# Optimization experiments

Hardware: AMD Instinct MI355X
Metric: run time of the kernel (lower is better)

The kernel has to match this reference:

```python
import jax, jax.numpy as jnp
import numpy as np

B, T, IN, OUT = 32, 1024, 1024, 1024
DT = 1.0
TAU_MIN, TAU_MAX = 5.0, 25.0


def setup_inputs() -> dict:
    key = jax.random.key(0)
    k1, k2, k3 = jax.random.split(key, 3)
    bound = 1.0 / np.sqrt(IN)
    inputs = jax.random.normal(k1, (B, T, IN), dtype=jnp.float32)
    weight = jax.random.uniform(k2, (OUT, IN), dtype=jnp.float32, minval=-bound, maxval=bound)
    bias = jnp.zeros((OUT,), dtype=jnp.float32)
    # per-neuron decay alpha = exp(-dt/tau), tau ~ U[tau_min, tau_max]
    tau = jax.random.uniform(k3, (OUT,), dtype=jnp.float32, minval=TAU_MIN, maxval=TAU_MAX)
    decay = jnp.exp(-DT / tau)
    return {"inputs": inputs, "weight": weight, "bias": bias, "decay": decay}


def reference(inputs, weight, bias, decay):
    # time-distributed linear projection: [B,T,IN] @ [OUT,IN]^T -> [B,T,OUT]
    current = jnp.einsum('bti,oi->bto', inputs, weight) + bias
    u0 = jnp.zeros((inputs.shape[0], weight.shape[0]), dtype=current.dtype)

    def step(u, x_t):
        # leaky integrator: u_t = alpha*u_{t-1} + (1-alpha)*x_t
        u = decay * u + (1.0 - decay) * x_t
        return u, u

    # scan over time: move T to leading axis
    _, u_seq = jax.lax.scan(step, u0, jnp.swapaxes(current, 0, 1))
    return jnp.swapaxes(u_seq, 0, 1)  # [B,T,OUT]
```

## Files before the change

kernel.cpp:

```cpp
#include <hip/hip_runtime.h>

#define M_DIM 32768
#define N_DIM 1024
#define K_DIM 1024
#define T_DIM 1024
#define B_DIM 32
#define NCHUNK 8
#define CHUNK_T 128

typedef unsigned int uint32;
typedef __attribute__((ext_vector_type(8))) short short8;
typedef __attribute__((ext_vector_type(8))) unsigned short ushort8v;
typedef __attribute__((ext_vector_type(4))) float floatx4;

__device__ __forceinline__ unsigned short f2bf(float f) {
    uint32 u = __float_as_uint(f);
    uint32 r = u + 0x7fffu + ((u >> 16) & 1u);
    return (unsigned short)(r >> 16);
}

__device__ __forceinline__ void async_load16(const void* g, void* s) {
    __builtin_amdgcn_global_load_lds(
        (const __attribute__((address_space(1))) void*)g,
        (__attribute__((address_space(3))) void*)s,
        16, 0, 0);
}

__global__ void cast_f32_bf16_x8(const float* __restrict__ src,
                                 unsigned short* __restrict__ dst, int n8) {
    int i = blockIdx.x * blockDim.x + threadIdx.x;
    if (i < n8) {
        const float4* s4 = (const float4*)src;
        float4 v0 = s4[(size_t)i * 2];
        float4 v1 = s4[(size_t)i * 2 + 1];
        ushort8v o;
        o[0] = f2bf(v0.x); o[1] = f2bf(v0.y); o[2] = f2bf(v0.z); o[3] = f2bf(v0.w);
        o[4] = f2bf(v1.x); o[5] = f2bf(v1.y); o[6] = f2bf(v1.z); o[7] = f2bf(v1.w);
        ((ushort8v*)dst)[i] = o;
    }
}

__global__ __launch_bounds__(512, 2) void gemm_8phase(
    const unsigned short* __restrict__ A,
    const unsigned short* __restrict__ Bw,
    const float* __restrict__ bias,
    unsigned short* __restrict__ outBf) {
    extern __shared__ __align__(16) unsigned short smem[];

    const int tid  = threadIdx.x;
    const int lane = tid & 63;
    const int wid  = tid >> 6;
    const int l15  = lane & 15;
    const int quad = lane >> 4;
    const int wm   = wid >> 2;
    const int wn   = wid & 3;

    const int L   = blockIdx.y * gridDim.x + blockIdx.x;
    const int xcd = L & 7;
    const int s   = L >> 3;
    const int bn0 = (s & 3) * 256;
    const int bm0 = (xcd * 16 + (s >> 2)) * 256;

    const int t3  = tid >> 3;
    const int sc8 = ((tid & 7) ^ (t3 & 7)) * 8;

#define STAGE_A(IH, T, PB) do {                                              \
        size_t kof_ = (size_t)(T) * 64 + sc8;                                \
        _Pragma("unroll") for (int q_ = 0; q_ < 2; ++q_) {                   \
            int ar_ = q_ * 128 + (IH) * 64 + t3;                             \
            int dr_ = q_ * 128 + (IH) * 64 + wid * 8;                        \
            async_load16(A + (size_t)(bm0 + ar_) * K_DIM + kof_,             \
                         smem + (PB) * 32768 + dr_ * 64);                    \
        } } while (0)
#define STAGE_B(JH, T, PB) do {                                              \
        size_t kof_ = (size_t)(T) * 64 + sc8;                                \
        _Pragma("unroll") for (int q_ = 0; q_ < 2; ++q_) {                   \
            int br_ = (q_ * 2 + (tid >> 8)) * 64 + (JH) * 32 + (t3 & 31);    \
            int dr_ = (q_ * 2 + (wid >> 2)) * 64 + (JH) * 32 + (wid & 3) * 8;\
            async_load16(Bw + (size_t)(bn0 + br_) * K_DIM + kof_,            \
                         smem + (PB) * 32768 + 16384 + dr_ * 64);            \
        } } while (0)

#define LD_A(IH) do {                                                        \
        const unsigned short* As_ = smem + pb * 32768;                       \
        _Pragma("unroll") for (int ii = 0; ii < 4; ++ii) {                   \
            int r_ = wm * 128 + (IH) * 64 + ii * 16 + l15;                   \
            _Pragma("unroll") for (int ks = 0; ks < 2; ++ks) {               \
                int c_ = ks * 4 + quad;                                      \
                af[ii][ks] = *(const short8*)&As_[r_ * 64 +                  \
                                                 ((c_ ^ (l15 & 7)) * 8)];    \
            } } } while (0)
#define LD_B(JH) do {                                                        \
        const unsigned short* Bs_ = smem + pb * 32768 + 16384;               \
        _Pragma("unroll") for (int jj = 0; jj < 2; ++jj) {                   \
            int r_ = wn * 64 + ((JH) * 2 + jj) * 16 + l15;                   \
            _Pragma("unroll") for (int ks = 0; ks < 2; ++ks) {               \
                int c_ = ks * 4 + quad;                                      \
                bfr[(JH) * 2 + jj][ks] = *(const short8*)&Bs_[r_ * 64 +      \
                                                 ((c_ ^ (l15 & 7)) * 8)];    \
            } } } while (0)
#define MM(IH, JH) do {                                                      \
        __builtin_amdgcn_s_setprio(1);                                       \
        _Pragma("unroll") for (int ii = 0; ii < 4; ++ii)                     \
        _Pragma("unroll") for (int jj = 0; jj < 2; ++jj)                     \
        _Pragma("unroll") for (int ks = 0; ks < 2; ++ks)                     \
            acc[(IH) * 4 + ii][(JH) * 2 + jj] =                              \
                __builtin_amdgcn_mfma_f32_16x16x32_bf16(                     \
                    af[ii][ks], bfr[(JH) * 2 + jj][ks],                      \
                    acc[(IH) * 4 + ii][(JH) * 2 + jj], 0, 0, 0);             \
        __builtin_amdgcn_s_setprio(0);                                       \
    } while (0)

#define FENCE  asm volatile("" ::: "memory")
#define BAR    __builtin_amdgcn_s_barrier()
#define LGKM0  asm volatile("s_waitcnt lgkmcnt(0)" ::: "memory")
#define SCHED0 __builtin_amdgcn_sched_barrier(0)

    floatx4 acc[8][4];
#pragma unroll
    for (int i = 0; i < 8; ++i)
#pragma unroll
        for (int j = 0; j < 4; ++j)
            acc[i][j] = (floatx4){0.f, 0.f, 0.f, 0.f};

    short8 af[4][2];
    short8 bfr[4][2];

    const int NT = K_DIM / 64;

    STAGE_A(0, 0, 0); STAGE_A(1, 0, 0); STAGE_B(0, 0, 0); STAGE_B(1, 0, 0);
    STAGE_A(0, 1, 1); STAGE_B(1, 1, 1); STAGE_B(0, 1, 1);
    asm volatile("s_waitcnt vmcnt(6)" ::: "memory");
    FENCE; BAR;

    for (int g = 0; g < NT; ++g) {
        const int pb = g & 1;
        const int po = pb ^ 1;

        LD_A(0); LD_B(0);
        if (g + 1 < NT) STAGE_A(1, g + 1, po);
        FENCE; BAR; LGKM0; SCHED0;
        MM(0, 0);
        SCHED0; FENCE; BAR;

        LD_B(1);
        if (g + 2 < NT) STAGE_A(0, g + 2, pb);
        FENCE; BAR; LGKM0; SCHED0;
        MM(0, 1);
        SCHED0; FENCE; BAR;

        LD_A(1);
        if (g + 2 < NT) STAGE_B(1, g + 2, pb);
        FENCE; BAR; LGKM0; SCHED0;
        MM(1, 0);
        SCHED0; FENCE; BAR;

        if (g + 2 < NT) STAGE_B(0, g + 2, pb);
        if (g < NT - 2) {
            asm volatile("s_waitcnt vmcnt(6)" ::: "memory");
        } else if (g == NT - 2) {
            asm volatile("s_waitcnt vmcnt(0)" ::: "memory");
        }
        FENCE; BAR; LGKM0; SCHED0;
        MM(1, 1);
        SCHED0; FENCE; BAR;
    }
    asm volatile("s_waitcnt vmcnt(0)" ::: "memory");

    float bb[4];
#pragma unroll
    for (int j = 0; j < 4; ++j) bb[j] = bias[bn0 + wn * 64 + j * 16 + l15];
#pragma unroll
    for (int i = 0; i < 8; ++i) {
        int rowb = bm0 + wm * 128 + i * 16 + quad * 4;
#pragma unroll
        for (int r = 0; r < 4; ++r) {
            size_t rb = (size_t)(rowb + r) * N_DIM + bn0 + wn * 64 + l15;
#pragma unroll
            for (int j = 0; j < 4; ++j)
                outBf[rb + j * 16] = f2bf(acc[i][j][r] + bb[j]);
        }
    }
#undef STAGE_A
#undef STAGE_B
#undef LD_A
#undef LD_B
#undef MM
#undef FENCE
#undef BAR
#undef LGKM0
#undef SCHED0
}

__global__ __launch_bounds__(256) void gemm_mfma(
    const unsigned short* __restrict__ A,
    const unsigned short* __restrict__ Bw,
    const float* __restrict__ bias,
    unsigned short* outBf,
    float* outF) {
    __shared__ unsigned short As[128 * 64];
    __shared__ unsigned short Bs[128 * 64];

    const int tid  = threadIdx.x;
    const int lane = tid & 63;
    const int wid  = tid >> 6;
    const int l15  = lane & 15;
    const int quad = lane >> 4;
    const int wm   = wid >> 1;
    const int wn   = wid & 1;

    const int L    = blockIdx.y * gridDim.x + blockIdx.x;
    const int xcd  = L & 7;
    const int s    = L >> 3;
    const int bn0  = (s & 7) * 128;
    const int bm0  = (xcd * 32 + (s >> 3)) * 128;

    floatx4 acc[4][4];
#pragma unroll
    for (int i = 0; i < 4; ++i)
#pragma unroll
        for (int j = 0; j < 4; ++j)
            acc[i][j] = (floatx4){0.f, 0.f, 0.f, 0.f};

    for (int kt = 0; kt < K_DIM / 64; ++kt) {
        const int k0 = kt * 64;
#pragma unroll
        for (int q = 0; q < 4; ++q) {
            int slot = q * 256 + tid;
            int row  = slot >> 3;
            int chq  = slot & 7;
            int scq  = chq ^ (row & 7);
            async_load16(A + (size_t)(bm0 + row) * K_DIM + k0 + scq * 8,
                         &As[(q * 256 + wid * 64) * 8]);
        }
#pragma unroll
        for (int q = 0; q < 4; ++q) {
            int slot = q * 256 + tid;
            int row  = slot >> 3;
            int chq  = slot & 7;
            int scq  = chq ^ (row & 7);
            async_load16(Bw + (size_t)(bn0 + row) * K_DIM + k0 + scq * 8,
                         &Bs[(q * 256 + wid * 64) * 8]);
        }
        __syncthreads();

#pragma unroll
        for (int ks = 0; ks < 2; ++ks) {
            short8 af[4], bfr[4];
#pragma unroll
            for (int i = 0; i < 4; ++i) {
                int r = wm * 64 + i * 16 + l15;
                int c = ks * 4 + quad;
                af[i] = *(const short8*)&As[r * 64 + ((c ^ (r & 7)) * 8)];
            }
#pragma unroll
            for (int j = 0; j < 4; ++j) {
                int r = wn * 64 + j * 16 + l15;
                int c = ks * 4 + quad;
                bfr[j] = *(const short8*)&Bs[r * 64 + ((c ^ (r & 7)) * 8)];
            }
#pragma unroll
            for (int i = 0; i < 4; ++i)
#pragma unroll
                for (int j = 0; j < 4; ++j)
                    acc[i][j] = __builtin_amdgcn_mfma_f32_16x16x32_bf16(
                        af[i], bfr[j], acc[i][j], 0, 0, 0);
        }
        __syncthreads();
    }

#pragma unroll
    for (int j = 0; j < 4; ++j) {
        int col = bn0 + wn * 64 + j * 16 + l15;
        float bb = bias[col];
#pragma unroll
        for (int i = 0; i < 4; ++i) {
            int rowb = bm0 + wm * 64 + i * 16 + quad * 4;
#pragma unroll
            for (int r = 0; r < 4; ++r) {
                float v = acc[i][j][r] + bb;
                size_t idx = (size_t)(rowb + r) * N_DIM + col;
                if (outBf) outBf[idx] = f2bf(v);
                else       outF[idx]  = v;
            }
        }
    }
}

__global__ __launch_bounds__(256) void scan_carry2(
    const uint32* __restrict__ cur32,
    const float* __restrict__ decay,
    float* __restrict__ carry) {
    int tid   = blockIdx.x * 256 + threadIdx.x;
    int o2    = tid & 511;
    int chunk = (tid >> 9) & (NCHUNK - 1);
    int b     = tid >> 12;
    int o     = o2 * 2;
    size_t base = ((size_t)b * T_DIM + (size_t)chunk * CHUNK_T) * (N_DIM / 2) + o2;
    float2 a2 = *(const float2*)&decay[o];
    float a0 = a2.x, a1 = a2.y;
    float c0 = 1.f - a0, c1 = 1.f - a1;
    float u0 = 0.f, u1 = 0.f;
    for (int t0 = 0; t0 < CHUNK_T; t0 += 32) {
        uint32 x[32];
#pragma unroll
        for (int k = 0; k < 32; ++k)
            x[k] = cur32[base + (size_t)(t0 + k) * (N_DIM / 2)];
#pragma unroll
        for (int k = 0; k < 32; ++k) {
            float lo = __uint_as_float(x[k] << 16);
            float hi = __uint_as_float(x[k] & 0xffff0000u);
            u0 = a0 * u0 + c0 * lo;
            u1 = a1 * u1 + c1 * hi;
        }
    }
    float2* cw = (float2*)&carry[((size_t)b * NCHUNK + chunk) * N_DIM + o];
    *cw = (float2){u0, u1};
}

__global__ __launch_bounds__(256) void scan_apply2(
    const uint32* __restrict__ cur32,
    const float* __restrict__ decay,
    const float* __restrict__ carry,
    float* __restrict__ out) {
    int tid   = blockIdx.x * 256 + threadIdx.x;
    int o2    = tid & 511;
    int chunk = (tid >> 9) & (NCHUNK - 1);
    int b     = tid >> 12;
    int o     = o2 * 2;
    size_t base = ((size_t)b * T_DIM + (size_t)chunk * CHUNK_T) * (N_DIM / 2) + o2;
    float2 a2 = *(const float2*)&decay[o];
    float a0 = a2.x, a1 = a2.y;
    float c0 = 1.f - a0, c1 = 1.f - a1;

    float A0 = a0, A1 = a1;
#pragma unroll
    for (int i = 0; i < 7; ++i) { A0 *= A0; A1 *= A1; }

    float u0 = 0.f, u1 = 0.f;
    const float* cb = carry + (size_t)b * NCHUNK * N_DIM + o;
    for (int i = 0; i < chunk; ++i) {
        float2 cv = *(const float2*)&cb[(size_t)i * N_DIM];
        u0 = cv.x + A0 * u0;
        u1 = cv.y + A1 * u1;
    }

    float2* out2 = (float2*)out;
    size_t obase = ((size_t)b * T_DIM + (size_t)chunk * CHUNK_T) * (N_DIM / 2) + o2;
    for (int t0 = 0; t0 < CHUNK_T; t0 += 32) {
        uint32 x[32];
#pragma unroll
        for (int k = 0; k < 32; ++k)
            x[k] = cur32[base + (size_t)(t0 + k) * (N_DIM / 2)];
#pragma unroll
        for (int k = 0; k < 32; ++k) {
            float lo = __uint_as_float(x[k] << 16);
            float hi = __uint_as_float(x[k] & 0xffff0000u);
            u0 = a0 * u0 + c0 * lo;
            u1 = a1 * u1 + c1 * hi;
            out2[obase + (size_t)(t0 + k) * (N_DIM / 2)] = (float2){u0, u1};
        }
    }
}

__global__ void scan_f32_inplace(float* __restrict__ buf,
                                 const float* __restrict__ decay) {
    int tid = blockIdx.x * 64 + threadIdx.x;
    int o = tid & (N_DIM - 1);
    size_t base = ((size_t)(tid >> 10) << 20) + o;
    float a = decay[o];
    float c = 1.f - a;
    float u = 0.f;
    for (int t0 = 0; t0 < 1024; t0 += 16) {
        float x[16];
#pragma unroll
        for (int k = 0; k < 16; ++k)
            x[k] = buf[base + (size_t)(t0 + k) * N_DIM];
#pragma unroll
        for (int k = 0; k < 16; ++k) {
            u = a * u + c * x[k];
            buf[base + (size_t)(t0 + k) * N_DIM] = u;
        }
    }
}

__global__ void gemm_naive(const float* __restrict__ X, const float* __restrict__ W,
                           const float* __restrict__ bias, float* __restrict__ out) {
    __shared__ float As[16][17], Bs[16][17];
    int tx = threadIdx.x, ty = threadIdx.y;
    int m0 = blockIdx.y * 16, n0 = blockIdx.x * 16;
    float acc = 0.f;
    for (int k0 = 0; k0 < K_DIM; k0 += 16) {
        As[ty][tx] = X[(size_t)(m0 + ty) * K_DIM + k0 + tx];
        Bs[ty][tx] = W[(size_t)(n0 + ty) * K_DIM + k0 + tx];
        __syncthreads();
#pragma unroll
        for (int kk = 0; kk < 16; ++kk) acc += As[ty][kk] * Bs[tx][kk];
        __syncthreads();
    }
    out[(size_t)(m0 + ty) * N_DIM + n0 + tx] = acc + bias[n0 + tx];
}

extern "C" void kernel_launch(void* const* d_in, const int* in_sizes, int n_in,
                              void* d_out, int out_size, void* d_ws, size_t ws_size,
                              hipStream_t stream) {
    const float* X     = (const float*)d_in[0];
    const float* Wt    = (const float*)d_in[1];
    const float* bias  = (const float*)d_in[2];
    const float* decay = (const float*)d_in[3];
    float* out = (float*)d_out;

    static bool big_lds_ok = [] {
        return hipFuncSetAttribute(reinterpret_cast<const void*>(gemm_8phase),
                                   hipFuncAttributeMaxDynamicSharedMemorySize,
                                   131072) == hipSuccess;
    }();

    const size_t A_bytes  = (size_t)M_DIM * K_DIM * 2;
    const size_t W_bytes  = (size_t)N_DIM * K_DIM * 2;
    const size_t C_bytes  = (size_t)M_DIM * N_DIM * 2;
    const size_t cr_bytes = (size_t)B_DIM * NCHUNK * N_DIM * 4;
    const size_t need_mid  = A_bytes + W_bytes;
    const size_t need_full = A_bytes + W_bytes + C_bytes + cr_bytes;

    if (ws_size >= need_full) {
        unsigned short* Abf = (unsigned short*)d_ws;
        unsigned short* Wbf = (unsigned short*)((char*)d_ws + A_bytes);
        unsigned short* Cbf = (unsigned short*)((char*)d_ws + A_bytes + W_bytes);
        float* carry = (float*)((char*)d_ws + A_bytes + W_bytes + C_bytes);
        cast_f32_bf16_x8<<<(M_DIM * K_DIM / 8 + 255) / 256, 256, 0, stream>>>(X, Abf, M_DIM * K_DIM / 8);
        cast_f32_bf16_x8<<<(N_DIM * K_DIM / 8 + 255) / 256, 256, 0, stream>>>(Wt, Wbf, N_DIM * K_DIM / 8);
        if (big_lds_ok) {
            gemm_8phase<<<dim3(4, 128), 512, 131072, stream>>>(Abf, Wbf, bias, Cbf);
        } else {
            gemm_mfma<<<dim3(N_DIM / 128, M_DIM / 128), 256, 0, stream>>>(Abf, Wbf, bias, Cbf, nullptr);
        }
        const int scan_threads = B_DIM * NCHUNK * N_DIM / 2;
        scan_carry2<<<scan_threads / 256, 256, 0, stream>>>((const uint32*)Cbf, decay, carry);
        scan_apply2<<<scan_threads / 256, 256, 0, stream>>>((const uint32*)Cbf, decay, carry, out);
    } else if (ws_size >= need_mid) {
        unsigned short* Abf = (unsigned short*)d_ws;
        unsigned short* Wbf = (unsigned short*)((char*)d_ws + A_bytes);
        cast_f32_bf16_x8<<<(M_DIM * K_DIM / 8 + 255) / 256, 256, 0, stream>>>(X, Abf, M_DIM * K_DIM / 8);
        cast_f32_bf16_x8<<<(N_DIM * K_DIM / 8 + 255) / 256, 256, 0, stream>>>(Wt, Wbf, N_DIM * K_DIM / 8);
        gemm_mfma<<<dim3(N_DIM / 128, M_DIM / 128), 256, 0, stream>>>(Abf, Wbf, bias, nullptr, out);
        scan_f32_inplace<<<512, 64, 0, stream>>>(out, decay);
    } else {
        gemm_naive<<<dim3(N_DIM / 16, M_DIM / 16), dim3(16, 16), 0, stream>>>(X, Wt, bias, out);
        scan_f32_inplace<<<512, 64, 0, stream>>>(out, decay);
    }
}
```

Before: 154.9 us.

## Fuse fp32-to-bf16 input cast into a triple-buffered GEMM reading fp32 activations

```diff
diff --git a/kernel.cpp b/kernel.cpp
--- a/kernel.cpp
+++ b/kernel.cpp
@@ -24,6 +24,15 @@
         (const __attribute__((address_space(1))) void*)g,
         (__attribute__((address_space(3))) void*)s,
         16, 0, 0);
+}
+
+__device__ __forceinline__ short8 pk8(float4 a, float4 b) {
+    union { short8 s; uint32 d[4]; } u;
+    asm("v_cvt_pk_bf16_f32 %0, %1, %2" : "=v"(u.d[0]) : "v"(a.x), "v"(a.y));
+    asm("v_cvt_pk_bf16_f32 %0, %1, %2" : "=v"(u.d[1]) : "v"(a.z), "v"(a.w));
+    asm("v_cvt_pk_bf16_f32 %0, %1, %2" : "=v"(u.d[2]) : "v"(b.x), "v"(b.y));
+    asm("v_cvt_pk_bf16_f32 %0, %1, %2" : "=v"(u.d[3]) : "v"(b.z), "v"(b.w));
+    return u.s;
 }
 
 __global__ void cast_f32_bf16_x8(const float* __restrict__ src,
@@ -38,6 +47,145 @@
         o[4] = f2bf(v1.x); o[5] = f2bf(v1.y); o[6] = f2bf(v1.z); o[7] = f2bf(v1.w);
         ((ushort8v*)dst)[i] = o;
     }
+}
+
+__global__ __launch_bounds__(512, 2) void gemm_f32a(
+    const float* __restrict__ X32,
+    const unsigned short* __restrict__ Bw,
+    const float* __restrict__ bias,
+    unsigned short* __restrict__ outBf) {
+    extern __shared__ __align__(16) char smemc[];
+
+    const int tid  = threadIdx.x;
+    const int lane = tid & 63;
+    const int wid  = tid >> 6;
+    const int l15  = lane & 15;
+    const int quad = lane >> 4;
+    const int wm   = wid >> 2;
+    const int wn   = wid & 3;
+
+    const int L   = blockIdx.y * gridDim.x + blockIdx.x;
+    const int xcd = L & 7;
+    const int s   = L >> 3;
+    const int bn0 = (s & 3) * 256;
+    const int bm0 = (xcd * 16 + (s >> 2)) * 256;
+
+#define STAGE_A_U(U, T, PB) do {                                             \
+        int row_ = (U) * 64 + (tid >> 3);                                    \
+        int sc_  = ((tid & 7) ^ (row_ & 7)) * 4;                             \
+        async_load16(X32 + (size_t)(bm0 + row_) * K_DIM + (T) * 32 + sc_,    \
+                     (float*)smemc + (PB) * 8192 + ((U) * 64 + wid * 8) * 32); \
+    } while (0)
+#define STAGE_B_U(U, T, PB) do {                                             \
+        int row_ = (U) * 128 + (tid >> 2);                                   \
+        int sc_  = ((tid & 3) ^ (row_ & 3)) * 8;                             \
+        async_load16(Bw + (size_t)(bn0 + row_) * K_DIM + (T) * 32 + sc_,     \
+                     (unsigned short*)(smemc + 98304) + (PB) * 8192 +        \
+                         ((U) * 128 + wid * 16) * 32);                       \
+    } while (0)
+
+#define LD_A(IH) do {                                                        \
+        const float* As_ = (const float*)smemc + pb * 8192;                  \
+        _Pragma("unroll") for (int ii = 0; ii < 4; ++ii) {                   \
+            int r_ = wm * 128 + (IH) * 64 + ii * 16 + l15;                   \
+            int k_ = l15 & 7;                                                \
+            int c0_ = quad * 2;                                              \
+            float4 F0 = *(const float4*)&As_[r_ * 32 + ((c0_ ^ k_) * 4)];    \
+            float4 F1 = *(const float4*)&As_[r_ * 32 + (((c0_ + 1) ^ k_) * 4)]; \
+            af[ii] = pk8(F0, F1);                                            \
+        } } while (0)
+#define LD_B() do {                                                          \
+        const unsigned short* Bs_ =                                          \
+            (const unsigned short*)(smemc + 98304) + pb * 8192;              \
+        _Pragma("unroll") for (int jj = 0; jj < 4; ++jj) {                   \
+            int r_ = wn * 64 + jj * 16 + l15;                                \
+            bfr[jj] = *(const short8*)&Bs_[r_ * 32 + ((quad ^ (l15 & 3)) * 8)]; \
+        } } while (0)
+#define MM(IH) do {                                                          \
+        __builtin_amdgcn_s_setprio(1);                                       \
+        _Pragma("unroll") for (int ii = 0; ii < 4; ++ii)                     \
+        _Pragma("unroll") for (int jj = 0; jj < 4; ++jj)                     \
+            acc[(IH) * 4 + ii][jj] =                                         \
+                __builtin_amdgcn_mfma_f32_16x16x32_bf16(                     \
+                    af[ii], bfr[jj], acc[(IH) * 4 + ii][jj], 0, 0, 0);       \
+        __builtin_amdgcn_s_setprio(0);                                       \
+    } while (0)
+
+#define FENCE  asm volatile("" ::: "memory")
+#define BAR    __builtin_amdgcn_s_barrier()
+#define LGKM0  asm volatile("s_waitcnt lgkmcnt(0)" ::: "memory")
+#define SCHED0 __builtin_amdgcn_sched_barrier(0)
+
+    floatx4 acc[8][4];
+#pragma unroll
+    for (int i = 0; i < 8; ++i)
+#pragma unroll
+        for (int j = 0; j < 4; ++j)
+            acc[i][j] = (floatx4){0.f, 0.f, 0.f, 0.f};
+
+    short8 af[4];
+    short8 bfr[4];
+
+    const int NT = K_DIM / 32;
+
+    STAGE_A_U(0, 0, 0); STAGE_A_U(1, 0, 0); STAGE_A_U(2, 0, 0); STAGE_A_U(3, 0, 0);
+    STAGE_B_U(0, 0, 0); STAGE_B_U(1, 0, 0);
+    STAGE_A_U(0, 1, 1); STAGE_A_U(1, 1, 1); STAGE_A_U(2, 1, 1); STAGE_A_U(3, 1, 1);
+    STAGE_B_U(0, 1, 1); STAGE_B_U(1, 1, 1);
+    asm volatile("s_waitcnt vmcnt(6)" ::: "memory");
+    FENCE; BAR;
+
+    int pb = 0;
+    for (int g = 0; g < NT; ++g) {
+        const int pn = (pb >= 1) ? pb - 1 : 2;
+
+        LD_A(0); LD_B();
+        if (g + 2 < NT) { STAGE_A_U(0, g + 2, pn); STAGE_A_U(1, g + 2, pn);
+                          STAGE_A_U(2, g + 2, pn); }
+        FENCE; BAR; LGKM0; SCHED0;
+        MM(0);
+        SCHED0; FENCE; BAR;
+
+        LD_A(1);
+        if (g + 2 < NT) { STAGE_A_U(3, g + 2, pn); STAGE_B_U(0, g + 2, pn);
+                          STAGE_B_U(1, g + 2, pn); }
+        if (g < NT - 2) {
+            asm volatile("s_waitcnt vmcnt(6)" ::: "memory");
+        } else if (g == NT - 2) {
+            asm volatile("s_waitcnt vmcnt(0)" ::: "memory");
+        }
+        FENCE; BAR; LGKM0; SCHED0;
+        MM(1);
+        SCHED0; FENCE; BAR;
+
+        pb = (pb == 2) ? 0 : pb + 1;
+    }
+    asm volatile("s_waitcnt vmcnt(0)" ::: "memory");
+
+    float bb[4];
+#pragma unroll
+    for (int j = 0; j < 4; ++j) bb[j] = bias[bn0 + wn * 64 + j * 16 + l15];
+    unsigned short* eb = (unsigned short*)smemc + wid * 2048;
+#pragma unroll
+    for (int i = 0; i < 8; ++i) {
+#pragma unroll
+        for (int j = 0; j < 4; ++j)
+#pragma unroll
+            for (int r = 0; r < 4; ++r)
+                eb[(quad * 4 + r) * 64 + j * 16 + l15] = f2bf(acc[i][j][r] + bb[j]);
+        asm volatile("s_waitcnt lgkmcnt(0)" ::: "memory");
+        short8 v0 = *(const short8*)&eb[lane * 8];
+        short8 v1 = *(const short8*)&eb[512 + lane * 8];
+        int rowg = bm0 + wm * 128 + i * 16 + (lane >> 3);
+        int colg = bn0 + wn * 64 + (lane & 7) * 8;
+        *(short8*)&outBf[(size_t)rowg * N_DIM + colg] = v0;
+        *(short8*)&outBf[(size_t)(rowg + 8) * N_DIM + colg] = v1;
+    }
+#undef STAGE_A_U
+#undef STAGE_B_U
+#undef LD_A
+#undef LD_B
+#undef MM
 }
 
 __global__ __launch_bounds__(512, 2) void gemm_8phase(
@@ -80,8 +228,7 @@
             async_load16(Bw + (size_t)(bn0 + br_) * K_DIM + kof_,            \
                          smem + (PB) * 32768 + 16384 + dr_ * 64);            \
         } } while (0)
-
-#define LD_A(IH) do {                                                        \
+#define LD_A8(IH) do {                                                       \
         const unsigned short* As_ = smem + pb * 32768;                       \
         _Pragma("unroll") for (int ii = 0; ii < 4; ++ii) {                   \
             int r_ = wm * 128 + (IH) * 64 + ii * 16 + l15;                   \
@@ -90,7 +237,7 @@
                 af[ii][ks] = *(const short8*)&As_[r_ * 64 +                  \
                                                  ((c_ ^ (l15 & 7)) * 8)];    \
             } } } while (0)
-#define LD_B(JH) do {                                                        \
+#define LD_B8(JH) do {                                                       \
         const unsigned short* Bs_ = smem + pb * 32768 + 16384;               \
         _Pragma("unroll") for (int jj = 0; jj < 2; ++jj) {                   \
             int r_ = wn * 64 + ((JH) * 2 + jj) * 16 + l15;                   \
@@ -99,7 +246,7 @@
                 bfr[(JH) * 2 + jj][ks] = *(const short8*)&Bs_[r_ * 64 +      \
                                                  ((c_ ^ (l15 & 7)) * 8)];    \
             } } } while (0)
-#define MM(IH, JH) do {                                                      \
+#define MM8(IH, JH) do {                                                     \
         __builtin_amdgcn_s_setprio(1);                                       \
         _Pragma("unroll") for (int ii = 0; ii < 4; ++ii)                     \
         _Pragma("unroll") for (int jj = 0; jj < 2; ++jj)                     \
@@ -111,11 +258,6 @@
         __builtin_amdgcn_s_setprio(0);                                       \
     } while (0)
 
-#define FENCE  asm volatile("" ::: "memory")
-#define BAR    __builtin_amdgcn_s_barrier()
-#define LGKM0  asm volatile("s_waitcnt lgkmcnt(0)" ::: "memory")
-#define SCHED0 __builtin_amdgcn_sched_barrier(0)
-
     floatx4 acc[8][4];
 #pragma unroll
     for (int i = 0; i < 8; ++i)
@@ -137,22 +279,22 @@
         const int pb = g & 1;
         const int po = pb ^ 1;
 
-        LD_A(0); LD_B(0);
+        LD_A8(0); LD_B8(0);
         if (g + 1 < NT) STAGE_A(1, g + 1, po);
         FENCE; BAR; LGKM0; SCHED0;
-        MM(0, 0);
+        MM8(0, 0);
         SCHED0; FENCE; BAR;
 
-        LD_B(1);
+        LD_B8(1);
         if (g + 2 < NT) STAGE_A(0, g + 2, pb);
         FENCE; BAR; LGKM0; SCHED0;
-        MM(0, 1);
+        MM8(0, 1);
         SCHED0; FENCE; BAR;
 
-        LD_A(1);
+        LD_A8(1);
         if (g + 2 < NT) STAGE_B(1, g + 2, pb);
         FENCE; BAR; LGKM0; SCHED0;
-        MM(1, 0);
+        MM8(1, 0);
         SCHED0; FENCE; BAR;
 
         if (g + 2 < NT) STAGE_B(0, g + 2, pb);
@@ -162,7 +304,7 @@
             asm volatile("s_waitcnt vmcnt(0)" ::: "memory");
         }
         FENCE; BAR; LGKM0; SCHED0;
-        MM(1, 1);
+        MM8(1, 1);
         SCHED0; FENCE; BAR;
     }
     asm volatile("s_waitcnt vmcnt(0)" ::: "memory");
@@ -183,108 +325,13 @@
     }
 #undef STAGE_A
 #undef STAGE_B
-#undef LD_A
-#undef LD_B
-#undef MM
+#undef LD_A8
+#undef LD_B8
+#undef MM8
 #undef FENCE
 #undef BAR
 #undef LGKM0
 #undef SCHED0
-}
-
-__global__ __launch_bounds__(256) void gemm_mfma(
-    const unsigned short* __restrict__ A,
-    const unsigned short* __restrict__ Bw,
-    const float* __restrict__ bias,
-    unsigned short* outBf,
-    float* outF) {
-    __shared__ unsigned short As[128 * 64];
-    __shared__ unsigned short Bs[128 * 64];
-
-    const int tid  = threadIdx.x;
-    const int lane = tid & 63;
-    const int wid  = tid >> 6;
-    const int l15  = lane & 15;
-    const int quad = lane >> 4;
-    const int wm   = wid >> 1;
-    const int wn   = wid & 1;
-
-    const int L    = blockIdx.y * gridDim.x + blockIdx.x;
-    const int xcd  = L & 7;
-    const int s    = L >> 3;
-    const int bn0  = (s & 7) * 128;
-    const int bm0  = (xcd * 32 + (s >> 3)) * 128;
-
-    floatx4 acc[4][4];
-#pragma unroll
-    for (int i = 0; i < 4; ++i)
-#pragma unroll
-        for (int j = 0; j < 4; ++j)
-            acc[i][j] = (floatx4){0.f, 0.f, 0.f, 0.f};
-
-    for (int kt = 0; kt < K_DIM / 64; ++kt) {
-        const int k0 = kt * 64;
-#pragma unroll
-        for (int q = 0; q < 4; ++q) {
-            int slot = q * 256 + tid;
-            int row  = slot >> 3;
-            int chq  = slot & 7;
-            int scq  = chq ^ (row & 7);
-            async_load16(A + (size_t)(bm0 + row) * K_DIM + k0 + scq * 8,
-                         &As[(q * 256 + wid * 64) * 8]);
-        }
-#pragma unroll
-        for (int q = 0; q < 4; ++q) {
-            int slot = q * 256 + tid;
-            int row  = slot >> 3;
-            int chq  = slot & 7;
-            int scq  = chq ^ (row & 7);
-            async_load16(Bw + (size_t)(bn0 + row) * K_DIM + k0 + scq * 8,
-                         &Bs[(q * 256 + wid * 64) * 8]);
-        }
-        __syncthreads();
-
-#pragma unroll
-        for (int ks = 0; ks < 2; ++ks) {
-            short8 af[4], bfr[4];
-#pragma unroll
-            for (int i = 0; i < 4; ++i) {
-                int r = wm * 64 + i * 16 + l15;
-                int c = ks * 4 + quad;
-                af[i] = *(const short8*)&As[r * 64 + ((c ^ (r & 7)) * 8)];
-            }
-#pragma unroll
-            for (int j = 0; j < 4; ++j) {
-                int r = wn * 64 + j * 16 + l15;
-                int c = ks * 4 + quad;
-                bfr[j] = *(const short8*)&Bs[r * 64 + ((c ^ (r & 7)) * 8)];
-            }
-#pragma unroll
-            for (int i = 0; i < 4; ++i)
-#pragma unroll
-                for (int j = 0; j < 4; ++j)
-                    acc[i][j] = __builtin_amdgcn_mfma_f32_16x16x32_bf16(
-                        af[i], bfr[j], acc[i][j], 0, 0, 0);
-        }
-        __syncthreads();
-    }
-
-#pragma unroll
-    for (int j = 0; j < 4; ++j) {
-        int col = bn0 + wn * 64 + j * 16 + l15;
-        float bb = bias[col];
-#pragma unroll
-        for (int i = 0; i < 4; ++i) {
-            int rowb = bm0 + wm * 64 + i * 16 + quad * 4;
-#pragma unroll
-            for (int r = 0; r < 4; ++r) {
-                float v = acc[i][j][r] + bb;
-                size_t idx = (size_t)(rowb + r) * N_DIM + col;
-                if (outBf) outBf[idx] = f2bf(v);
-                else       outF[idx]  = v;
-            }
-        }
-    }
 }
 
 __global__ __launch_bounds__(256) void scan_carry2(
@@ -384,6 +431,101 @@
     }
 }
 
+__global__ __launch_bounds__(256) void gemm_mfma(
+    const unsigned short* __restrict__ A,
+    const unsigned short* __restrict__ Bw,
+    const float* __restrict__ bias,
+    unsigned short* outBf,
+    float* outF) {
+    __shared__ unsigned short As[128 * 64];
+    __shared__ unsigned short Bs[128 * 64];
+
+    const int tid  = threadIdx.x;
+    const int lane = tid & 63;
+    const int wid  = tid >> 6;
+    const int l15  = lane & 15;
+    const int quad = lane >> 4;
+    const int wm   = wid >> 1;
+    const int wn   = wid & 1;
+
+    const int L    = blockIdx.y * gridDim.x + blockIdx.x;
+    const int xcd  = L & 7;
+    const int s    = L >> 3;
+    const int bn0  = (s & 7) * 128;
+    const int bm0  = (xcd * 32 + (s >> 3)) * 128;
+
+    floatx4 acc[4][4];
+#pragma unroll
+    for (int i = 0; i < 4; ++i)
+#pragma unroll
+        for (int j = 0; j < 4; ++j)
+            acc[i][j] = (floatx4){0.f, 0.f, 0.f, 0.f};
+
+    for (int kt = 0; kt < K_DIM / 64; ++kt) {
+        const int k0 = kt * 64;
+#pragma unroll
+        for (int q = 0; q < 4; ++q) {
+            int slot = q * 256 + tid;
+            int row  = slot >> 3;
+            int chq  = slot & 7;
+            int scq  = chq ^ (row & 7);
+            async_load16(A + (size_t)(bm0 + row) * K_DIM + k0 + scq * 8,
+                         &As[(q * 256 + wid * 64) * 8]);
+        }
+#pragma unroll
+        for (int q = 0; q < 4; ++q) {
+            int slot = q * 256 + tid;
+            int row  = slot >> 3;
+            int chq  = slot & 7;
+            int scq  = chq ^ (row & 7);
+            async_load16(Bw + (size_t)(bn0 + row) * K_DIM + k0 + scq * 8,
+                         &Bs[(q * 256 + wid * 64) * 8]);
+        }
+        __syncthreads();
+
+#pragma unroll
+        for (int ks = 0; ks < 2; ++ks) {
+            short8 af[4], bfr[4];
+#pragma unroll
+            for (int i = 0; i < 4; ++i) {
+                int r = wm * 64 + i * 16 + l15;
+                int c = ks * 4 + quad;
+                af[i] = *(const short8*)&As[r * 64 + ((c ^ (r & 7)) * 8)];
+            }
+#pragma unroll
+            for (int j = 0; j < 4; ++j) {
+                int r = wn * 64 + j * 16 + l15;
+                int c = ks * 4 + quad;
+                bfr[j] = *(const short8*)&Bs[r * 64 + ((c ^ (r & 7)) * 8)];
+            }
+#pragma unroll
+            for (int i = 0; i < 4; ++i)
+#pragma unroll
+                for (int j = 0; j < 4; ++j)
+                    acc[i][j] = __builtin_amdgcn_mfma_f32_16x16x32_bf16(
+                        af[i], bfr[j], acc[i][j], 0, 0, 0);
+        }
+        __syncthreads();
+    }
+
+#pragma unroll
+    for (int j = 0; j < 4; ++j) {
+        int col = bn0 + wn * 64 + j * 16 + l15;
+        float bb = bias[col];
+#pragma unroll
+        for (int i = 0; i < 4; ++i) {
+            int rowb = bm0 + wm * 64 + i * 16 + quad * 4;
+#pragma unroll
+            for (int r = 0; r < 4; ++r) {
+                float v = acc[i][j][r] + bb;
+                size_t idx = (size_t)(rowb + r) * N_DIM + col;
+                if (outBf) outBf[idx] = f2bf(v);
+                else       outF[idx]  = v;
+            }
+        }
+    }
+}
+
 __global__ void gemm_naive(const float* __restrict__ X, const float* __restrict__ W,
                            const float* __restrict__ bias, float* __restrict__ out) {
     __shared__ float As[16][17], Bs[16][17];
@@ -410,7 +552,12 @@
     const float* decay = (const float*)d_in[3];
     float* out = (float*)d_out;
 
-    static bool big_lds_ok = [] {
+    static bool lds144_ok = [] {
+        return hipFuncSetAttribute(reinterpret_cast<const void*>(gemm_f32a),
+                                   hipFuncAttributeMaxDynamicSharedMemorySize,
+                                   147456) == hipSuccess;
+    }();
+    static bool lds128_ok = [] {
         return hipFuncSetAttribute(reinterpret_cast<const void*>(gemm_8phase),
                                    hipFuncAttributeMaxDynamicSharedMemorySize,
                                    131072) == hipSuccess;
@@ -420,22 +567,27 @@
     const size_t W_bytes  = (size_t)N_DIM * K_DIM * 2;
     const size_t C_bytes  = (size_t)M_DIM * N_DIM * 2;
     const size_t cr_bytes = (size_t)B_DIM * NCHUNK * N_DIM * 4;
+    const size_t need_new  = W_bytes + C_bytes + cr_bytes;
     const size_t need_mid  = A_bytes + W_bytes;
     const size_t need_full = A_bytes + W_bytes + C_bytes + cr_bytes;
-
-    if (ws_size >= need_full) {
+    const int scan_threads = B_DIM * NCHUNK * N_DIM / 2;
+
+    if (lds144_ok && ws_size >= need_new) {
+        unsigned short* Wbf = (unsigned short*)d_ws;
+        unsigned short* Cbf = (unsigned short*)((char*)d_ws + W_bytes);
+        float* carry = (float*)((char*)d_ws + W_bytes + C_bytes);
+        cast_f32_bf16_x8<<<(N_DIM * K_DIM / 8 + 255) / 256, 256, 0, stream>>>(Wt, Wbf, N_DIM * K_DIM / 8);
+        gemm_f32a<<<dim3(4, 128), 512, 147456, stream>>>(X, Wbf, bias, Cbf);
+        scan_carry2<<<scan_threads / 256, 256, 0, stream>>>((const uint32*)Cbf, decay, carry);
+        scan_apply2<<<scan_threads / 256, 256, 0, stream>>>((const uint32*)Cbf, decay, carry, out);
+    } else if (lds128_ok && ws_size >= need_full) {
         unsigned short* Abf = (unsigned short*)d_ws;
         unsigned short* Wbf = (unsigned short*)((char*)d_ws + A_bytes);
         unsigned short* Cbf = (unsigned short*)((char*)d_ws + A_bytes + W_bytes);
         float* carry = (float*)((char*)d_ws + A_bytes + W_bytes + C_bytes);
         cast_f32_bf16_x8<<<(M_DIM * K_DIM / 8 + 255) / 256, 256, 0, stream>>>(X, Abf, M_DIM * K_DIM / 8);
         cast_f32_bf16_x8<<<(N_DIM * K_DIM / 8 + 255) / 256, 256, 0, stream>>>(Wt, Wbf, N_DIM * K_DIM / 8);
-        if (big_lds_ok) {
-            gemm_8phase<<<dim3(4, 128), 512, 131072, stream>>>(Abf, Wbf, bias, Cbf);
-        } else {
-            gemm_mfma<<<dim3(N_DIM / 128, M_DIM / 128), 256, 0, stream>>>(Abf, Wbf, bias, Cbf, nullptr);
-        }
-        const int scan_threads = B_DIM * NCHUNK * N_DIM / 2;
+        gemm_8phase<<<dim3(4, 128), 512, 131072, stream>>>(Abf, Wbf, bias, Cbf);
         scan_carry2<<<scan_threads / 256, 256, 0, stream>>>((const uint32*)Cbf, decay, carry);
         scan_apply2<<<scan_threads / 256, 256, 0, stream>>>((const uint32*)Cbf, decay, carry, out);
     } else if (ws_size >= need_mid) {
```

Measured after the change: 174.8 us. +12.8%, slower.

## Fuse fp32-to-bf16 activation cast into GEMM A-tile staging

Applied to the files above, without the earlier changes.

```diff
diff --git a/kernel.cpp b/kernel.cpp
--- a/kernel.cpp
+++ b/kernel.cpp
@@ -25,6 +25,74 @@
         (__attribute__((address_space(3))) void*)s,
         16, 0, 0);
 }
+
+__device__ __forceinline__ short8 pk8(floatx4 a, floatx4 b) {
+    union { short8 s; uint32 d[4]; } u;
+    asm("v_cvt_pk_bf16_f32 %0, %1, %2" : "=v"(u.d[0]) : "v"(a[0]), "v"(a[1]));
+    asm("v_cvt_pk_bf16_f32 %0, %1, %2" : "=v"(u.d[1]) : "v"(a[2]), "v"(a[3]));
+    asm("v_cvt_pk_bf16_f32 %0, %1, %2" : "=v"(u.d[2]) : "v"(b[0]), "v"(b[1]));
+    asm("v_cvt_pk_bf16_f32 %0, %1, %2" : "=v"(u.d[3]) : "v"(b[2]), "v"(b[3]));
+    return u.s;
+}
+
+#define FENCE  asm volatile("" ::: "memory")
+#define BAR    __builtin_amdgcn_s_barrier()
+#define LGKM0  asm volatile("s_waitcnt lgkmcnt(0)" ::: "memory")
+#define SCHED0 __builtin_amdgcn_sched_barrier(0)
+#define VMW(N) asm volatile("s_waitcnt vmcnt(" #N ")" ::: "memory")
+
+#define STAGE_B(JH, T, PB) do {                                              \
+        size_t kof_ = (size_t)(T) * 64 + sc8;                                \
+        _Pragma("unroll") for (int q_ = 0; q_ < 2; ++q_) {                   \
+            int br_ = (q_ * 2 + (tid >> 8)) * 64 + (JH) * 32 + (t3 & 31);    \
+            int dr_ = (q_ * 2 + (wid >> 2)) * 64 + (JH) * 32 + (wid & 3) * 8;\
+            async_load16(Bw + (size_t)(bn0 + br_) * K_DIM + kof_,            \
+                         smem + (PB) * 32768 + 16384 + dr_ * 64);            \
+        } } while (0)
+
+#define LD_A8(IH) do {                                                       \
+        const unsigned short* As_ = smem + pb * 32768;                       \
+        _Pragma("unroll") for (int ii = 0; ii < 4; ++ii) {                   \
+            int r_ = wm * 128 + (IH) * 64 + ii * 16 + l15;                   \
+            _Pragma("unroll") for (int ks = 0; ks < 2; ++ks) {               \
+                int c_ = ks * 4 + quad;                                      \
+                af[ii][ks] = *(const short8*)&As_[r_ * 64 +                  \
+                                                 ((c_ ^ (l15 & 7)) * 8)];    \
+            } } } while (0)
+#define LD_B8(JH) do {                                                       \
+        const unsigned short* Bs_ = smem + pb * 32768 + 16384;               \
+        _Pragma("unroll") for (int jj = 0; jj < 2; ++jj) {                   \
+            int r_ = wn * 64 + ((JH) * 2 + jj) * 16 + l15;                   \
+            _Pragma("unroll") for (int ks = 0; ks < 2; ++ks) {               \
+                int c_ = ks * 4 + quad;                                      \
+                bfr[(JH) * 2 + jj][ks] = *(const short8*)&Bs_[r_ * 64 +      \
+                                                 ((c_ ^ (l15 & 7)) * 8)];    \
+            } } } while (0)
+#define MM8(IH, JH) do {                                                     \
+        __builtin_amdgcn_s_setprio(1);                                       \
+        _Pragma("unroll") for (int ii = 0; ii < 4; ++ii)                     \
+        _Pragma("unroll") for (int jj = 0; jj < 2; ++jj)                     \
+        _Pragma("unroll") for (int ks = 0; ks < 2; ++ks)                     \
+            acc[(IH) * 4 + ii][(JH) * 2 + jj] =                              \
+                __builtin_amdgcn_mfma_f32_16x16x32_bf16(                     \
+                    af[ii][ks], bfr[(JH) * 2 + jj][ks],                      \
+                    acc[(IH) * 4 + ii][(JH) * 2 + jj], 0, 0, 0);             \
+        __builtin_amdgcn_s_setprio(0);                                       \
+    } while (0)
+
+#define AISSUE(P, T) do {                                                    \
+        const float* p_ = abase[P] + (T) * 64;                               \
+        asm volatile("global_load_dwordx4 %0, %1, off"                       \
+                     : "=&v"(ar[2 * (P)]) : "v"(p_));                        \
+        asm volatile("global_load_dwordx4 %0, %1, off offset:16"             \
+                     : "=&v"(ar[2 * (P) + 1]) : "v"(p_));                    \
+    } while (0)
+#define AWRITE(P, PBDST) do {                                                \
+        int row_ = (P) * 64 + (tid >> 3);                                    \
+        int cs_  = (tid & 7) ^ (row_ & 7);                                   \
+        *(short8*)&smem[(PBDST) * 32768 + row_ * 64 + cs_ * 8] =             \
+            pk8(ar[2 * (P)], ar[2 * (P) + 1]);                               \
+    } while (0)
 
 __global__ void cast_f32_bf16_x8(const float* __restrict__ src,
                                  unsigned short* __restrict__ dst, int n8) {
@@ -40,6 +108,111 @@
     }
 }
 
+__global__ __launch_bounds__(512, 2) void gemm_fused(
+    const float* __restrict__ X32,
+    const unsigned short* __restrict__ Bw,
+    const float* __restrict__ bias,
+    unsigned short* __restrict__ outBf) {
+    extern __shared__ __align__(16) unsigned short smem[];
+
+    const int tid  = threadIdx.x;
+    const int lane = tid & 63;
+    const int wid  = tid >> 6;
+    const int l15  = lane & 15;
+    const int quad = lane >> 4;
+    const int wm   = wid >> 2;
+    const int wn   = wid & 3;
+
+    const int L   = blockIdx.y * gridDim.x + blockIdx.x;
+    const int xcd = L & 7;
+    const int s   = L >> 3;
+    const int bn0 = (s & 3) * 256;
+    const int bm0 = (xcd * 16 + (s >> 2)) * 256;
+
+    const int t3  = tid >> 3;
+    const int sc8 = ((tid & 7) ^ (t3 & 7)) * 8;
+
+    const float* abase[4];
+#pragma unroll
+    for (int p = 0; p < 4; ++p)
+        abase[p] = X32 + (size_t)(bm0 + p * 64 + (tid >> 3)) * K_DIM + (tid & 7) * 8;
+
+    floatx4 acc[8][4];
+#pragma unroll
+    for (int i = 0; i < 8; ++i)
+#pragma unroll
+        for (int j = 0; j < 4; ++j)
+            acc[i][j] = (floatx4){0.f, 0.f, 0.f, 0.f};
+
+    short8 af[4][2];
+    short8 bfr[4][2];
+    floatx4 ar[8];
+
+    AISSUE(0, 0); AISSUE(1, 0); AISSUE(2, 0); AISSUE(3, 0);
+    STAGE_B(0, 0, 0); STAGE_B(1, 0, 0);
+    VMW(2); SCHED0;
+    AWRITE(0, 0); AWRITE(1, 0); AWRITE(2, 0); AWRITE(3, 0);
+    AISSUE(0, 1); STAGE_B(0, 1, 1); AISSUE(1, 1); AISSUE(2, 1);
+    STAGE_B(1, 1, 1); AISSUE(3, 1);
+    VMW(10); LGKM0; FENCE; BAR;
+
+#define TILE_MAIN(G) do {                                                    \
+        const int pb = (G) & 1;                                              \
+        LD_A8(0); LD_B8(0);                                                  \
+        VMW(8); SCHED0; AWRITE(0, pb ^ 1); AISSUE(0, (G) + 2);               \
+        LGKM0; BAR; SCHED0; MM8(0, 0); BAR;                                  \
+        LD_B8(1); STAGE_B(0, (G) + 2, pb);                                   \
+        VMW(8); SCHED0; AWRITE(1, pb ^ 1); AISSUE(1, (G) + 2);               \
+        LGKM0; BAR; SCHED0; MM8(0, 1); BAR;                                  \
+        LD_A8(1);                                                            \
+        VMW(8); SCHED0; AWRITE(2, pb ^ 1); AISSUE(2, (G) + 2);               \
+        LGKM0; BAR; SCHED0; MM8(1, 0); BAR;                                  \
+        STAGE_B(1, (G) + 2, pb);                                             \
+        VMW(8); SCHED0; AWRITE(3, pb ^ 1); AISSUE(3, (G) + 2);               \
+        LGKM0; BAR; SCHED0; MM8(1, 1); BAR;                                  \
+    } while (0)
+
+    for (int g = 0; g < 14; ++g) TILE_MAIN(g);
+
+    {
+        const int pb = 0;
+        LD_A8(0); LD_B8(0);
+        VMW(8); SCHED0; AWRITE(0, 1);
+        LGKM0; BAR; SCHED0; MM8(0, 0); BAR;
+        LD_B8(1);
+        VMW(5); SCHED0; AWRITE(1, 1);
+        LGKM0; BAR; SCHED0; MM8(0, 1); BAR;
+        LD_A8(1);
+        VMW(3); SCHED0; AWRITE(2, 1);
+        LGKM0; BAR; SCHED0; MM8(1, 0); BAR;
+        VMW(0); SCHED0; AWRITE(3, 1);
+        LGKM0; BAR; SCHED0; MM8(1, 1); BAR;
+    }
+    {
+        const int pb = 1;
+        LD_A8(0); LD_B8(0); LGKM0; BAR; SCHED0; MM8(0, 0); BAR;
+        LD_B8(1);           LGKM0; BAR; SCHED0; MM8(0, 1); BAR;
+        LD_A8(1);           LGKM0; BAR; SCHED0; MM8(1, 0); BAR;
+                            LGKM0; BAR; SCHED0; MM8(1, 1); BAR;
+    }
+#undef TILE_MAIN
+
+    float bb[4];
+#pragma unroll
+    for (int j = 0; j < 4; ++j) bb[j] = bias[bn0 + wn * 64 + j * 16 + l15];
+#pragma unroll
+    for (int i = 0; i < 8; ++i) {
+        int rowb = bm0 + wm * 128 + i * 16 + quad * 4;
+#pragma unroll
+        for (int r = 0; r < 4; ++r) {
+            size_t rb = (size_t)(rowb + r) * N_DIM + bn0 + wn * 64 + l15;
+#pragma unroll
+            for (int j = 0; j < 4; ++j)
+                outBf[rb + j * 16] = f2bf(acc[i][j][r] + bb[j]);
+        }
+    }
+}
+
 __global__ __launch_bounds__(512, 2) void gemm_8phase(
     const unsigned short* __restrict__ A,
     const unsigned short* __restrict__ Bw,
@@ -72,49 +245,6 @@
             async_load16(A + (size_t)(bm0 + ar_) * K_DIM + kof_,             \
                          smem + (PB) * 32768 + dr_ * 64);                    \
         } } while (0)
-#define STAGE_B(JH, T, PB) do {                                              \
-        size_t kof_ = (size_t)(T) * 64 + sc8;                                \
-        _Pragma("unroll") for (int q_ = 0; q_ < 2; ++q_) {                   \
-            int br_ = (q_ * 2 + (tid >> 8)) * 64 + (JH) * 32 + (t3 & 31);    \
-            int dr_ = (q_ * 2 + (wid >> 2)) * 64 + (JH) * 32 + (wid & 3) * 8;\
-            async_load16(Bw + (size_t)(bn0 + br_) * K_DIM + kof_,            \
-                         smem + (PB) * 32768 + 16384 + dr_ * 64);            \
-        } } while (0)
-
-#define LD_A(IH) do {                                                        \
-        const unsigned short* As_ = smem + pb * 32768;                       \
-        _Pragma("unroll") for (int ii = 0; ii < 4; ++ii) {                   \
-            int r_ = wm * 128 + (IH) * 64 + ii * 16 + l15;                   \
-            _Pragma("unroll") for (int ks = 0; ks < 2; ++ks) {               \
-                int c_ = ks * 4 + quad;                                      \
-                af[ii][ks] = *(const short8*)&As_[r_ * 64 +                  \
-                                                 ((c_ ^ (l15 & 7)) * 8)];    \
-            } } } while (0)
-#define LD_B(JH) do {                                                        \
-        const unsigned short* Bs_ = smem + pb * 32768 + 16384;               \
-        _Pragma("unroll") for (int jj = 0; jj < 2; ++jj) {                   \
-            int r_ = wn * 64 + ((JH) * 2 + jj) * 16 + l15;                   \
-            _Pragma("unroll") for (int ks = 0; ks < 2; ++ks) {               \
-                int c_ = ks * 4 + quad;                                      \
-                bfr[(JH) * 2 + jj][ks] = *(const short8*)&Bs_[r_ * 64 +      \
-                                                 ((c_ ^ (l15 & 7)) * 8)];    \
-            } } } while (0)
-#define MM(IH, JH) do {                                                      \
-        __builtin_amdgcn_s_setprio(1);                                       \
-        _Pragma("unroll") for (int ii = 0; ii < 4; ++ii)                     \
-        _Pragma("unroll") for (int jj = 0; jj < 2; ++jj)                     \
-        _Pragma("unroll") for (int ks = 0; ks < 2; ++ks)                     \
-            acc[(IH) * 4 + ii][(JH) * 2 + jj] =                              \
-                __builtin_amdgcn_mfma_f32_16x16x32_bf16(                     \
-                    af[ii][ks], bfr[(JH) * 2 + jj][ks],                      \
-                    acc[(IH) * 4 + ii][(JH) * 2 + jj], 0, 0, 0);             \
-        __builtin_amdgcn_s_setprio(0);                                       \
-    } while (0)
-
-#define FENCE  asm volatile("" ::: "memory")
-#define BAR    __builtin_amdgcn_s_barrier()
-#define LGKM0  asm volatile("s_waitcnt lgkmcnt(0)" ::: "memory")
-#define SCHED0 __builtin_amdgcn_sched_barrier(0)
 
     floatx4 acc[8][4];
 #pragma unroll
@@ -137,22 +267,22 @@
         const int pb = g & 1;
         const int po = pb ^ 1;
 
-        LD_A(0); LD_B(0);
+        LD_A8(0); LD_B8(0);
         if (g + 1 < NT) STAGE_A(1, g + 1, po);
         FENCE; BAR; LGKM0; SCHED0;
-        MM(0, 0);
+        MM8(0, 0);
         SCHED0; FENCE; BAR;
 
-        LD_B(1);
+        LD_B8(1);
         if (g + 2 < NT) STAGE_A(0, g + 2, pb);
         FENCE; BAR; LGKM0; SCHED0;
-        MM(0, 1);
+        MM8(0, 1);
         SCHED0; FENCE; BAR;
 
-        LD_A(1);
+        LD_A8(1);
         if (g + 2 < NT) STAGE_B(1, g + 2, pb);
         FENCE; BAR; LGKM0; SCHED0;
-        MM(1, 0);
+        MM8(1, 0);
         SCHED0; FENCE; BAR;
 
         if (g + 2 < NT) STAGE_B(0, g + 2, pb);
@@ -162,7 +292,7 @@
             asm volatile("s_waitcnt vmcnt(0)" ::: "memory");
         }
         FENCE; BAR; LGKM0; SCHED0;
-        MM(1, 1);
+        MM8(1, 1);
         SCHED0; FENCE; BAR;
     }
     asm volatile("s_waitcnt vmcnt(0)" ::: "memory");
@@ -182,109 +312,6 @@
         }
     }
 #undef STAGE_A
-#undef STAGE_B
-#undef LD_A
-#undef LD_B
-#undef MM
-#undef FENCE
-#undef BAR
-#undef LGKM0
-#undef SCHED0
-}
-
-__global__ __launch_bounds__(256) void gemm_mfma(
-    const unsigned short* __restrict__ A,
-    const unsigned short* __restrict__ Bw,
-    const float* __restrict__ bias,
-    unsigned short* outBf,
-    float* outF) {
-    __shared__ unsigned short As[128 * 64];
-    __shared__ unsigned short Bs[128 * 64];
-
-    const int tid  = threadIdx.x;
-    const int lane = tid & 63;
-    const int wid  = tid >> 6;
-    const int l15  = lane & 15;
-    const int quad = lane >> 4;
-    const int wm   = wid >> 1;
-    const int wn   = wid & 1;
-
-    const int L    = blockIdx.y * gridDim.x + blockIdx.x;
-    const int xcd  = L & 7;
-    const int s    = L >> 3;
-    const int bn0  = (s & 7) * 128;
-    const int bm0  = (xcd * 32 + (s >> 3)) * 128;
-
-    floatx4 acc[4][4];
-#pragma unroll
-    for (int i = 0; i < 4; ++i)
-#pragma unroll
-        for (int j = 0; j < 4; ++j)
-            acc[i][j] = (floatx4){0.f, 0.f, 0.f, 0.f};
-
-    for (int kt = 0; kt < K_DIM / 64; ++kt) {
-        const int k0 = kt * 64;
-#pragma unroll
-        for (int q = 0; q < 4; ++q) {
-            int slot = q * 256 + tid;
-            int row  = slot >> 3;
-            int chq  = slot & 7;
-            int scq  = chq ^ (row & 7);
-            async_load16(A + (size_t)(bm0 + row) * K_DIM + k0 + scq * 8,
-                         &As[(q * 256 + wid * 64) * 8]);
-        }
-#pragma unroll
-        for (int q = 0; q < 4; ++q) {
-            int slot = q * 256 + tid;
-            int row  = slot >> 3;
-            int chq  = slot & 7;
-            int scq  = chq ^ (row & 7);
-            async_load16(Bw + (size_t)(bn0 + row) * K_DIM + k0 + scq * 8,
-                         &Bs[(q * 256 + wid * 64) * 8]);
-        }
-        __syncthreads();
-
-#pragma unroll
-        for (int ks = 0; ks < 2; ++ks) {
-            short8 af[4], bfr[4];
-#pragma unroll
-            for (int i = 0; i < 4; ++i) {
-                int r = wm * 64 + i * 16 + l15;
-                int c = ks * 4 + quad;
-                af[i] = *(const short8*)&As[r * 64 + ((c ^ (r & 7)) * 8)];
-            }
-#pragma unroll
-            for (int j = 0; j < 4; ++j) {
-                int r = wn * 64 + j * 16 + l15;
-                int c = ks * 4 + quad;
-                bfr[j] = *(const short8*)&Bs[r * 64 + ((c ^ (r & 7)) * 8)];
-            }
-#pragma unroll
-            for (int i = 0; i < 4; ++i)
-#pragma unroll
-                for (int j = 0; j < 4; ++j)
-                    acc[i][j] = __builtin_amdgcn_mfma_f32_16x16x32_bf16(
-                        af[i], bfr[j], acc[i][j], 0, 0, 0);
-        }
-        __syncthreads();
-    }
-
-#pragma unroll
-    for (int j = 0; j < 4; ++j) {
-        int col = bn0 + wn * 64 + j * 16 + l15;
-        float bb = bias[col];
-#pragma unroll
-        for (int i = 0; i < 4; ++i) {
-            int rowb = bm0 + wm * 64 + i * 16 + quad * 4;
-#pragma unroll
-            for (int r = 0; r < 4; ++r) {
-                float v = acc[i][j][r] + bb;
-                size_t idx = (size_t)(rowb + r) * N_DIM + col;
-                if (outBf) outBf[idx] = f2bf(v);
-                else       outF[idx]  = v;
-            }
-        }
-    }
 }
 
 __global__ __launch_bounds__(256) void scan_carry2(
@@ -384,6 +411,101 @@
     }
 }
 
+__global__ __launch_bounds__(256) void gemm_mfma(
+    const unsigned short* __restrict__ A,
+    const unsigned short* __restrict__ Bw,
+    const float* __restrict__ bias,
+    unsigned short* outBf,
+    float* outF) {
+    __shared__ unsigned short As[128 * 64];
+    __shared__ unsigned short Bs[128 * 64];
+
+    const int tid  = threadIdx.x;
+    const int lane = tid & 63;
+    const int wid  = tid >> 6;
+    const int l15  = lane & 15;
+    const int quad = lane >> 4;
+    const int wm   = wid >> 1;
+    const int wn   = wid & 1;
+
+    const int L    = blockIdx.y * gridDim.x + blockIdx.x;
+    const int xcd  = L & 7;
+    const int s    = L >> 3;
+    const int bn0  = (s & 7) * 128;
+    const int bm0  = (xcd * 32 + (s >> 3)) * 128;
+
+    floatx4 acc[4][4];
+#pragma unroll
+    for (int i = 0; i < 4; ++i)
+#pragma unroll
+        for (int j = 0; j < 4; ++j)
+            acc[i][j] = (floatx4){0.f, 0.f, 0.f, 0.f};
+
+    for (int kt = 0; kt < K_DIM / 64; ++kt) {
+        const int k0 = kt * 64;
+#pragma unroll
+        for (int q = 0; q < 4; ++q) {
+            int slot = q * 256 + tid;
+            int row  = slot >> 3;
+            int chq  = slot & 7;
+            int scq  = chq ^ (row & 7);
+            async_load16(A + (size_t)(bm0 + row) * K_DIM + k0 + scq * 8,
+                         &As[(q * 256 + wid * 64) * 8]);
+        }
+#pragma unroll
+        for (int q = 0; q < 4; ++q) {
+            int slot = q * 256 + tid;
+            int row  = slot >> 3;
+            int chq  = slot & 7;
+            int scq  = chq ^ (row & 7);
+            async_load16(Bw + (size_t)(bn0 + row) * K_DIM + k0 + scq * 8,
+                         &Bs[(q * 256 + wid * 64) * 8]);
+        }
+        __syncthreads();
+
+#pragma unroll
+        for (int ks = 0; ks < 2; ++ks) {
+            short8 af[4], bfr[4];
+#pragma unroll
+            for (int i = 0; i < 4; ++i) {
+                int r = wm * 64 + i * 16 + l15;
+                int c = ks * 4 + quad;
+                af[i] = *(const short8*)&As[r * 64 + ((c ^ (r & 7)) * 8)];
+            }
+#pragma unroll
+            for (int j = 0; j < 4; ++j) {
+                int r = wn * 64 + j * 16 + l15;
+                int c = ks * 4 + quad;
+                bfr[j] = *(const short8*)&Bs[r * 64 + ((c ^ (r & 7)) * 8)];
+            }
+#pragma unroll
+            for (int i = 0; i < 4; ++i)
+#pragma unroll
+                for (int j = 0; j < 4; ++j)
+                    acc[i][j] = __builtin_amdgcn_mfma_f32_16x16x32_bf16(
+                        af[i], bfr[j], acc[i][j], 0, 0, 0);
+        }
+        __syncthreads();
+    }
+
+#pragma unroll
+    for (int j = 0; j < 4; ++j) {
+        int col = bn0 + wn * 64 + j * 16 + l15;
+        float bb = bias[col];
+#pragma unroll
+        for (int i = 0; i < 4; ++i) {
+            int rowb = bm0 + wm * 64 + i * 16 + quad * 4;
+#pragma unroll
+            for (int r = 0; r < 4; ++r) {
+                float v = acc[i][j][r] + bb;
+                size_t idx = (size_t)(rowb + r) * N_DIM + col;
+                if (outBf) outBf[idx] = f2bf(v);
+                else       outF[idx]  = v;
+            }
+        }
+    }
+}
+
 __global__ void gemm_naive(const float* __restrict__ X, const float* __restrict__ W,
                            const float* __restrict__ bias, float* __restrict__ out) {
     __shared__ float As[16][17], Bs[16][17];
@@ -410,7 +532,12 @@
     const float* decay = (const float*)d_in[3];
     float* out = (float*)d_out;
 
-    static bool big_lds_ok = [] {
+    static bool fused_ok = [] {
+        return hipFuncSetAttribute(reinterpret_cast<const void*>(gemm_fused),
+                                   hipFuncAttributeMaxDynamicSharedMemorySize,
+                                   131072) == hipSuccess;
+    }();
+    static bool lds128_ok = [] {
         return hipFuncSetAttribute(reinterpret_cast<const void*>(gemm_8phase),
                                    hipFuncAttributeMaxDynamicSharedMemorySize,
                                    131072) == hipSuccess;
@@ -420,22 +547,27 @@
     const size_t W_bytes  = (size_t)N_DIM * K_DIM * 2;
     const size_t C_bytes  = (size_t)M_DIM * N_DIM * 2;
     const size_t cr_bytes = (size_t)B_DIM * NCHUNK * N_DIM * 4;
+    const size_t need_new  = W_bytes + C_bytes + cr_bytes;
     const size_t need_mid  = A_bytes + W_bytes;
     const size_t need_full = A_bytes + W_bytes + C_bytes + cr_bytes;
-
-    if (ws_size >= need_full) {
+    const int scan_threads = B_DIM * NCHUNK * N_DIM / 2;
+
+    if (fused_ok && ws_size >= need_new) {
+        unsigned short* Wbf = (unsigned short*)d_ws;
+        unsigned short* Cbf = (unsigned short*)((char*)d_ws + W_bytes);
+        float* carry = (float*)((char*)d_ws + W_bytes + C_bytes);
+        cast_f32_bf16_x8<<<(N_DIM * K_DIM / 8 + 255) / 256, 256, 0, stream>>>(Wt, Wbf, N_DIM * K_DIM / 8);
+        gemm_fused<<<dim3(4, 128), 512, 131072, stream>>>(X, Wbf, bias, Cbf);
+        scan_carry2<<<scan_threads / 256, 256, 0, stream>>>((const uint32*)Cbf, decay, carry);
+        scan_apply2<<<scan_threads / 256, 256, 0, stream>>>((const uint32*)Cbf, decay, carry, out);
+    } else if (lds128_ok && ws_size >= need_full) {
         unsigned short* Abf = (unsigned short*)d_ws;
         unsigned short* Wbf = (unsigned short*)((char*)d_ws + A_bytes);
         unsigned short* Cbf = (unsigned short*)((char*)d_ws + A_bytes + W_bytes);
         float* carry = (float*)((char*)d_ws + A_bytes + W_bytes + C_bytes);
         cast_f32_bf16_x8<<<(M_DIM * K_DIM / 8 + 255) / 256, 256, 0, stream>>>(X, Abf, M_DIM * K_DIM / 8);
         cast_f32_bf16_x8<<<(N_DIM * K_DIM / 8 + 255) / 256, 256, 0, stream>>>(Wt, Wbf, N_DIM * K_DIM / 8);
-        if (big_lds_ok) {
-            gemm_8phase<<<dim3(4, 128), 512, 131072, stream>>>(Abf, Wbf, bias, Cbf);
-        } else {
-            gemm_mfma<<<dim3(N_DIM / 128, M_DIM / 128), 256, 0, stream>>>(Abf, Wbf, bias, Cbf, nullptr);
-        }
-        const int scan_threads = B_DIM * NCHUNK * N_DIM / 2;
+        gemm_8phase<<<dim3(4, 128), 512, 131072, stream>>>(Abf, Wbf, bias, Cbf);
         scan_carry2<<<scan_threads / 256, 256, 0, stream>>>((const uint32*)Cbf, decay, carry);
         scan_apply2<<<scan_threads / 256, 256, 0, stream>>>((const uint32*)Cbf, decay, carry, out);
     } else if (ws_size >= need_mid) {
```

New measurement: 153.8 us. Within noise of the previous version (-0.7%).
